# Kernel tuning notes

Hardware: AMD Instinct MI355X
Metric: run time of the kernel (lower is better)

Reference implementation:

```python
import jax, jax.numpy as jnp
import numpy as np

EPS = 1e-5
H = 16  # num_heads


def _ln(x, s, b):
    m = x.mean(-1, keepdims=True)
    v = x.var(-1, keepdims=True)
    return (x - m) / jnp.sqrt(v + EPS) * s + b


def _gru_gate(x, y, W, U, bg):
    # W, U: [3, D, D] stacked (Wr, Wz, Wg) / (Ur, Uz, Ug); torch Linear: a @ W.T
    r = jax.nn.sigmoid(y @ W[0].T + x @ U[0].T)
    z = jax.nn.sigmoid(y @ W[1].T + x @ U[1].T - bg)
    h = jnp.tanh(y @ W[2].T + (r * x) @ U[2].T)
    return (1.0 - z) * x + z * h


def setup_inputs() -> dict:
    N, L, D = 4, 1024, 1024
    hs = D // H
    rng = jax.random.key(0)
    ks = iter(jax.random.split(rng, 24))

    def xav(shape):
        sc = float(np.sqrt(2.0 / (shape[-1] + shape[-2])))
        return jax.random.normal(next(ks), shape, jnp.float32) * sc

    inp = {
        'value': jax.random.normal(next(ks), (N, L, D), jnp.float32),
        'key': jax.random.normal(next(ks), (N, L, D), jnp.float32),
        'query': jax.random.normal(next(ks), (N, L, D), jnp.float32),
        'mask': jax.random.randint(next(ks), (N, L), 0, 2).astype(jnp.int32),
        # shared-head QKV projections (head_size x head_size)
        'wq': xav((hs, hs)), 'wk': xav((hs, hs)), 'wv': xav((hs, hs)),
        'w_out': xav((D, D)), 'b_out': jnp.zeros((D,), jnp.float32),
        'fc_w': xav((D, D)), 'fc_b': jnp.zeros((D,), jnp.float32),
        'ln1_s': jnp.ones((D,), jnp.float32), 'ln1_b': jnp.zeros((D,), jnp.float32),
        'lnkv_s': jnp.ones((D,), jnp.float32), 'lnkv_b': jnp.zeros((D,), jnp.float32),
        'ln2_s': jnp.ones((D,), jnp.float32), 'ln2_b': jnp.zeros((D,), jnp.float32),
        'g1_W': xav((3, D, D)), 'g1_U': xav((3, D, D)), 'g1_bg': jnp.full((D,), 2.0, jnp.float32),
        'g2_W': xav((3, D, D)), 'g2_U': xav((3, D, D)), 'g2_bg': jnp.full((D,), 2.0, jnp.float32),
    }
    return inp


def reference(value, key, query, mask, wq, wk, wv, w_out, b_out, fc_w, fc_b,
              ln1_s, ln1_b, lnkv_s, lnkv_b, ln2_s, ln2_b,
              g1_W, g1_U, g1_bg, g2_W, g2_U, g2_bg):
    N, L, D = query.shape
    hs = D // H
    # pre-LN: query normed with norm1, value normed with norm_kv; key := normed value
    q_ = _ln(query, ln1_s, ln1_b)
    v_ = _ln(value, lnkv_s, lnkv_b)
    k_ = v_
    # shared per-head projections: [N, L, H, hs] @ W.T
    qh = q_.reshape(N, L, H, hs) @ wq.T
    kh = k_.reshape(N, L, H, hs) @ wk.T
    vh = v_.reshape(N, L, H, hs) @ wv.T
    energy = jnp.einsum('nqhd,nkhd->nhqk', qh, kh)
    energy = jnp.where(mask[:, None, None, :] == 0, jnp.float32(-1e20), energy)
    # NOTE: original scales by sqrt(embed_dim), not sqrt(head_size)
    attn = jax.nn.softmax(energy / jnp.sqrt(jnp.float32(D)), axis=-1)
    o = jnp.einsum('nhqk,nkhd->nqhd', attn, vh).reshape(N, L, D) @ w_out.T + b_out
    # GRU-gated residuals (GTrXL)
    h = _gru_gate(query, o, g1_W, g1_U, g1_bg)
    h_ = _ln(h, ln2_s, ln2_b)
    f = jax.nn.relu(h_ @ fc_w.T + fc_b)
    out = _gru_gate(h, f, g2_W, g2_U, g2_bg)
    return out, attn
```

## Files before the change

kernel.cpp:

```cpp
#include <hip/hip_runtime.h>
#include <cstdint>
#include <cstddef>

#define N_ 4
#define L_ 1024
#define D_ 1024
#define H_ 16
#define HS_ 64
#define M_ (N_*L_)
#define DD_ (D_*D_)

typedef unsigned short u16;
typedef __bf16 b16x8 __attribute__((ext_vector_type(8)));
typedef float f32x4 __attribute__((ext_vector_type(4)));

__device__ __forceinline__ float sigmoidf_(float x) { return 1.0f / (1.0f + __expf(-x)); }
__device__ __forceinline__ u16 f2bf(float f) {
    union { float f; uint32_t u; } c; c.f = f;
    uint32_t u = c.u;
    u += 0x7fffu + ((u >> 16) & 1u);
    return (u16)(u >> 16);
}

__device__ __forceinline__ void gl_lds16(const void* g, void* l) {
    auto gp = reinterpret_cast<const __attribute__((address_space(1))) unsigned int*>(
        reinterpret_cast<uintptr_t>(g));
    auto lp = reinterpret_cast<__attribute__((address_space(3))) unsigned int*>(
        reinterpret_cast<uintptr_t>(l));
    __builtin_amdgcn_global_load_lds(gp, lp, 16, 0, 0);
}

__global__ __launch_bounds__(256) void prep_weights_kernel(
    const float* __restrict__ w_out, const float* __restrict__ fc_w,
    const float* __restrict__ wq, const float* __restrict__ wk, const float* __restrict__ wv,
    const float* __restrict__ g1W, const float* __restrict__ g1U,
    const float* __restrict__ g2W, const float* __restrict__ g2U,
    u16* __restrict__ ws0) {
    u16* Wop = ws0;
    u16* Wfc = ws0 + (size_t)DD_;
    u16* WQKV = ws0 + 2 * (size_t)DD_;
    u16* G1rz = WQKV + 16384;
    u16* G1h = G1rz + 4 * (size_t)DD_;
    u16* G2rz = G1h + 2 * (size_t)DD_;
    u16* G2h = G2rz + 4 * (size_t)DD_;
    int b = blockIdx.x, t = threadIdx.x;
    const float* src; u16* dst; size_t si, di;
    if (b < 512) {
        size_t f = (size_t)b * 2048 + t * 8; src = w_out; si = f; dst = Wop; di = f;
    } else if (b < 1024) {
        size_t f = (size_t)(b - 512) * 2048 + t * 8; src = fc_w; si = f; dst = Wfc; di = f;
    } else if (b < 1030) {
        size_t f = (size_t)(b - 1024) * 2048 + t * 8;
        int which = (int)(f >> 12); size_t off = f & 4095;
        src = which == 0 ? wq : (which == 1 ? wk : wv); si = off; dst = WQKV; di = f;
    } else if (b < 3078) {
        size_t f = (size_t)(b - 1030) * 2048 + t * 8;
        size_t row = f >> 11, k = f & 2047; size_t n2 = (row >= 1024) ? 1 : 0;
        src = (k < 1024) ? (g1W + n2 * DD_) : (g1U + n2 * DD_);
        si = (row & 1023) * 1024 + (k & 1023); dst = G1rz; di = f;
    } else if (b < 4102) {
        size_t f = (size_t)(b - 3078) * 2048 + t * 8;
        size_t row = f >> 11, k = f & 2047;
        src = (k < 1024) ? (g1W + 2 * (size_t)DD_) : (g1U + 2 * (size_t)DD_);
        si = row * 1024 + (k & 1023); dst = G1h; di = f;
    } else if (b < 6150) {
        size_t f = (size_t)(b - 4102) * 2048 + t * 8;
        size_t row = f >> 11, k = f & 2047; size_t n2 = (row >= 1024) ? 1 : 0;
        src = (k < 1024) ? (g2W + n2 * DD_) : (g2U + n2 * DD_);
        si = (row & 1023) * 1024 + (k & 1023); dst = G2rz; di = f;
    } else {
        size_t f = (size_t)(b - 6150) * 2048 + t * 8;
        size_t row = f >> 11, k = f & 2047;
        src = (k < 1024) ? (g2W + 2 * (size_t)DD_) : (g2U + 2 * (size_t)DD_);
        si = row * 1024 + (k & 1023); dst = G2h; di = f;
    }
    float4 a = *(const float4*)&src[si];
    float4 b4 = *(const float4*)&src[si + 4];
    u16 o[8] = { f2bf(a.x), f2bf(a.y), f2bf(a.z), f2bf(a.w),
                 f2bf(b4.x), f2bf(b4.y), f2bf(b4.z), f2bf(b4.w) };
    *(uint4*)&dst[di] = *(uint4*)o;
}

__global__ __launch_bounds__(256) void ln_kernel(const float* __restrict__ x, u16* __restrict__ y,
                                                 const float* __restrict__ sc, const float* __restrict__ bi) {
    int row = blockIdx.x;
    const float* xr = x + (size_t)row * D_;
    int t = threadIdx.x;
    float4 v = *(const float4*)&xr[t * 4];
    float s = v.x + v.y + v.z + v.w;
    float q = v.x * v.x + v.y * v.y + v.z * v.z + v.w * v.w;
#pragma unroll
    for (int o = 32; o > 0; o >>= 1) { s += __shfl_xor(s, o); q += __shfl_xor(q, o); }
    __shared__ float ss[4], sq[4];
    int w = t >> 6;
    if ((t & 63) == 0) { ss[w] = s; sq[w] = q; }
    __syncthreads();
    s = ss[0] + ss[1] + ss[2] + ss[3];
    q = sq[0] + sq[1] + sq[2] + sq[3];
    float mean = s * (1.0f / D_);
    float var = q * (1.0f / D_) - mean * mean;
    float inv = rsqrtf(var + 1e-5f);
    float4 sv = *(const float4*)&sc[t * 4];
    float4 bv = *(const float4*)&bi[t * 4];
    u16 ov[4] = { f2bf((v.x - mean) * inv * sv.x + bv.x),
                  f2bf((v.y - mean) * inv * sv.y + bv.y),
                  f2bf((v.z - mean) * inv * sv.z + bv.z),
                  f2bf((v.w - mean) * inv * sv.w + bv.w) };
    *(ushort4*)&y[(size_t)row * D_ + t * 4] = *(ushort4*)ov;
}

__global__ __launch_bounds__(256) void proj_mfma_kernel(const u16* __restrict__ qbf,
                                                        const u16* __restrict__ vbf,
                                                        const u16* __restrict__ wqkv,
                                                        u16* __restrict__ qh, u16* __restrict__ kh,
                                                        u16* __restrict__ vt) {
    int t = threadIdx.x, w = t >> 6, l = t & 63;
    int lr = l & 15, lg = l >> 4;
    int rb = blockIdx.x, h = blockIdx.y;
    int n = rb >> 3, lbase = (rb & 7) * 128;
    const u16* wqp = wqkv;
    const u16* wkp = wqkv + 4096;
    const u16* wvp = wqkv + 8192;
    b16x8 wqf[4][2], wkf[4][2], wvf[4][2];
#pragma unroll
    for (int dt = 0; dt < 4; ++dt)
#pragma unroll
        for (int ks = 0; ks < 2; ++ks) {
            int a = (dt * 16 + lr) * 64 + ks * 32 + lg * 8;
            wqf[dt][ks] = *(const b16x8*)&wqp[a];
            wkf[dt][ks] = *(const b16x8*)&wkp[a];
            wvf[dt][ks] = *(const b16x8*)&wvp[a];
        }
#pragma unroll
    for (int rr = 0; rr < 2; ++rr) {
        int rt = w * 2 + rr;
        size_t grow = (size_t)(n * 1024 + lbase + rt * 16 + lr);
        b16x8 aq[2], av[2];
#pragma unroll
        for (int ks = 0; ks < 2; ++ks) {
            aq[ks] = *(const b16x8*)&qbf[grow * D_ + h * 64 + ks * 32 + lg * 8];
            av[ks] = *(const b16x8*)&vbf[grow * D_ + h * 64 + ks * 32 + lg * 8];
        }
#pragma unroll
        for (int dt = 0; dt < 4; ++dt) {
            f32x4 cq = (f32x4){0.f, 0.f, 0.f, 0.f};
            f32x4 ck = (f32x4){0.f, 0.f, 0.f, 0.f};
            f32x4 cv = (f32x4){0.f, 0.f, 0.f, 0.f};
            cq = __builtin_amdgcn_mfma_f32_16x16x32_bf16(aq[0], wqf[dt][0], cq, 0, 0, 0);
            cq = __builtin_amdgcn_mfma_f32_16x16x32_bf16(aq[1], wqf[dt][1], cq, 0, 0, 0);
            ck = __builtin_amdgcn_mfma_f32_16x16x32_bf16(av[0], wkf[dt][0], ck, 0, 0, 0);
            ck = __builtin_amdgcn_mfma_f32_16x16x32_bf16(av[1], wkf[dt][1], ck, 0, 0, 0);
            cv = __builtin_amdgcn_mfma_f32_16x16x32_bf16(wvf[dt][0], av[0], cv, 0, 0, 0);
            cv = __builtin_amdgcn_mfma_f32_16x16x32_bf16(wvf[dt][1], av[1], cv, 0, 0, 0);
#pragma unroll
            for (int r = 0; r < 4; ++r) {
                size_t orow = (size_t)(n * 1024 + lbase + rt * 16 + lg * 4 + r);
                qh[orow * D_ + h * 64 + dt * 16 + lr] = f2bf(cq[r]);
                kh[orow * D_ + h * 64 + dt * 16 + lr] = f2bf(ck[r]);
                vt[((size_t)(n * H_ + h) * 64 + dt * 16 + lg * 4 + r) * L_ + lbase + rt * 16 + lr] = f2bf(cv[r]);
            }
        }
    }
}

__global__ __launch_bounds__(512, 2) void qk_softmax_kernel(const u16* __restrict__ qh,
                                                            const u16* __restrict__ kh,
                                                            const int* __restrict__ mask,
                                                            float* __restrict__ attn) {
    int t = threadIdx.x;
    int w = t >> 6, l = t & 63;
    int qsub = w & 1, kq = w >> 1;
    int q0 = blockIdx.x * 32;
    int h = blockIdx.y, n = blockIdx.z;
    int lr = l & 15, lg = l >> 4;

    size_t qrow = ((size_t)(n * L_ + q0 + qsub * 16 + lr) * H_ + h) * HS_;
    b16x8 aq0 = *(const b16x8*)&qh[qrow + lg * 8];
    b16x8 aq1 = *(const b16x8*)&qh[qrow + 32 + lg * 8];

    f32x4 c[16];
#pragma unroll
    for (int i = 0; i < 16; ++i) c[i] = (f32x4){0.f, 0.f, 0.f, 0.f};

    size_t kbase = ((size_t)(n * L_ + kq * 256 + lr) * H_ + h) * HS_ + lg * 8;
#pragma unroll
    for (int kt = 0; kt < 16; ++kt) {
        const u16* kp = &kh[kbase + (size_t)kt * 16 * D_];
        b16x8 bk0 = *(const b16x8*)&kp[0];
        b16x8 bk1 = *(const b16x8*)&kp[32];
        c[kt] = __builtin_amdgcn_mfma_f32_16x16x32_bf16(aq0, bk0, c[kt], 0, 0, 0);
        c[kt] = __builtin_amdgcn_mfma_f32_16x16x32_bf16(aq1, bk1, c[kt], 0, 0, 0);
    }

    const float scl = 0.03125f;
    int kcol = kq * 256 + lr;
    float rowmax[4] = { -1e30f, -1e30f, -1e30f, -1e30f };
#pragma unroll
    for (int kt = 0; kt < 16; ++kt) {
        int mk = mask[n * L_ + kcol + kt * 16];
#pragma unroll
        for (int r = 0; r < 4; ++r) {
            float s = (mk != 0) ? c[kt][r] * scl : -1e20f;
            c[kt][r] = s;
            rowmax[r] = fmaxf(rowmax[r], s);
        }
    }
#pragma unroll
    for (int o = 8; o > 0; o >>= 1)
#pragma unroll
        for (int r = 0; r < 4; ++r) rowmax[r] = fmaxf(rowmax[r], __shfl_xor(rowmax[r], o));

    __shared__ float redA[32][4];
    __shared__ float redB[32][4];
    int qrow4 = qsub * 16 + lg * 4;
    if (lr == 0) {
#pragma unroll
        for (int r = 0; r < 4; ++r) redA[qrow4 + r][kq] = rowmax[r];
    }
    __syncthreads();
#pragma unroll
    for (int r = 0; r < 4; ++r)
        rowmax[r] = fmaxf(fmaxf(redA[qrow4 + r][0], redA[qrow4 + r][1]),
                          fmaxf(redA[qrow4 + r][2], redA[qrow4 + r][3]));
    float rowsum[4] = { 0.f, 0.f, 0.f, 0.f };
#pragma unroll
    for (int kt = 0; kt < 16; ++kt)
#pragma unroll
        for (int r = 0; r < 4; ++r) {
            float e = __expf(c[kt][r] - rowmax[r]);
            c[kt][r] = e;
            rowsum[r] += e;
        }
#pragma unroll
    for (int o = 8; o > 0; o >>= 1)
#pragma unroll
        for (int r = 0; r < 4; ++r) rowsum[r] += __shfl_xor(rowsum[r], o);
    if (lr == 0) {
#pragma unroll
        for (int r = 0; r < 4; ++r) redB[qrow4 + r][kq] = rowsum[r];
    }
    __syncthreads();
    float inv[4];
#pragma unroll
    for (int r = 0; r < 4; ++r)
        inv[r] = 1.0f / (redB[qrow4 + r][0] + redB[qrow4 + r][1] +
                         redB[qrow4 + r][2] + redB[qrow4 + r][3]);

    float* ap = attn + ((size_t)((n * H_ + h) * L_) + q0 + qrow4) * L_ + kcol;
#pragma unroll
    for (int kt = 0; kt < 16; ++kt)
#pragma unroll
        for (int r = 0; r < 4; ++r)
            ap[(size_t)r * L_ + kt * 16] = c[kt][r] * inv[r];
}

#define PLD 40
__global__ __launch_bounds__(256) void pv_mfma_kernel(const float* __restrict__ attn,
                                                      const u16* __restrict__ vt,
                                                      u16* __restrict__ o) {
    __shared__ u16 a_lds[128 * PLD];
    __shared__ u16 v_lds[64 * PLD];
    int t = threadIdx.x, w = t >> 6, l = t & 63;
    int lr = l & 15, lg = l >> 4;
    int qb = blockIdx.x * 128, h = blockIdx.y, n = blockIdx.z;
    const float* abase = attn + ((size_t)((n * H_ + h) * L_) + qb) * L_;
    const u16* vbase = vt + (size_t)(n * H_ + h) * HS_ * L_;
    f32x4 acc[4][2];
#pragma unroll
    for (int i = 0; i < 4; ++i)
#pragma unroll
        for (int j = 0; j < 2; ++j) acc[i][j] = (f32x4){0.f, 0.f, 0.f, 0.f};

    int sq = t >> 1, sk = (t & 1) * 16;
    int vd = t >> 2, vk = (t & 3) * 8;
    for (int kb = 0; kb < L_; kb += 32) {
        float va[16];
#pragma unroll
        for (int i = 0; i < 4; ++i)
            *(float4*)&va[i * 4] = *(const float4*)&abase[(size_t)sq * L_ + kb + sk + i * 4];
        b16x8 vv = *(const b16x8*)&vbase[(size_t)vd * L_ + kb + vk];
        u16 ua[16];
#pragma unroll
        for (int i = 0; i < 16; ++i) ua[i] = f2bf(va[i]);
        __syncthreads();
        *(uint4*)&a_lds[sq * PLD + sk] = *(uint4*)&ua[0];
        *(uint4*)&a_lds[sq * PLD + sk + 8] = *(uint4*)&ua[8];
        *(b16x8*)&v_lds[vd * PLD + vk] = vv;
        __syncthreads();
        b16x8 bq[2];
#pragma unroll
        for (int qt = 0; qt < 2; ++qt)
            bq[qt] = *(const b16x8*)&a_lds[(w * 32 + qt * 16 + lr) * PLD + lg * 8];
#pragma unroll
        for (int dt = 0; dt < 4; ++dt) {
            b16x8 av = *(const b16x8*)&v_lds[(dt * 16 + lr) * PLD + lg * 8];
#pragma unroll
            for (int qt = 0; qt < 2; ++qt)
                acc[dt][qt] = __builtin_amdgcn_mfma_f32_16x16x32_bf16(av, bq[qt], acc[dt][qt], 0, 0, 0);
        }
    }
#pragma unroll
    for (int dt = 0; dt < 4; ++dt)
#pragma unroll
        for (int qt = 0; qt < 2; ++qt) {
            int q = qb + w * 32 + qt * 16 + lr;
            int d = dt * 16 + lg * 4;
            u16 ov[4] = { f2bf(acc[dt][qt][0]), f2bf(acc[dt][qt][1]),
                          f2bf(acc[dt][qt][2]), f2bf(acc[dt][qt][3]) };
            *(ushort4*)&o[((size_t)(n * L_ + q) * H_ + h) * HS_ + d] = *(ushort4*)ov;
        }
}

__global__ __launch_bounds__(256) void gemm_bf16_kernel(const u16* __restrict__ A, int lda,
                                                        const u16* __restrict__ Bw, int ldb,
                                                        const float* __restrict__ bias,
                                                        float* __restrict__ C0, float* __restrict__ C1,
                                                        u16* __restrict__ Cbf, int ldc,
                                                        int K, int relu) {
    __shared__ u16 As[2][128 * 64];
    __shared__ u16 Bs[2][128 * 64];
    int t = threadIdx.x, w = t >> 6, l = t & 63;
    int wr = w >> 1, wc = w & 1;
    int m0 = blockIdx.x * 128, n0 = blockIdx.y * 128;
    int fr = l & 15, fq = l >> 4;
    int srow = l >> 3;
    int gc8 = (l & 7) ^ (srow & 7);
    const u16* Abase = A + (size_t)m0 * lda;
    const u16* Bbase = Bw + (size_t)n0 * ldb;

    f32x4 acc[4][4];
#pragma unroll
    for (int i = 0; i < 4; ++i)
#pragma unroll
        for (int j = 0; j < 4; ++j) acc[i][j] = (f32x4){0.f, 0.f, 0.f, 0.f};

    auto STAGE = [&](int buf, int kk) {
#pragma unroll
        for (int i = 0; i < 4; ++i) {
            int r0 = (i * 4 + w) * 8;
            gl_lds16(&Abase[(size_t)(r0 + srow) * lda + kk + gc8 * 8], &As[buf][r0 * 64]);
            gl_lds16(&Bbase[(size_t)(r0 + srow) * ldb + kk + gc8 * 8], &Bs[buf][r0 * 64]);
        }
    };
    STAGE(0, 0);
    const int NT = K >> 6;
    for (int kt = 0; kt < NT; ++kt) {
        int cur = kt & 1;
        if (kt + 1 < NT) {
            STAGE(cur ^ 1, (kt + 1) << 6);
            asm volatile("s_waitcnt vmcnt(8)" ::: "memory");
        } else {
            asm volatile("s_waitcnt vmcnt(0)" ::: "memory");
        }
        __builtin_amdgcn_s_barrier();
#pragma unroll
        for (int ks = 0; ks < 2; ++ks) {
            b16x8 af[4], bf[4];
#pragma unroll
            for (int i = 0; i < 4; ++i) {
                int row = wr * 64 + i * 16 + fr;
                af[i] = *(const b16x8*)&As[cur][row * 64 + (((ks * 4 + fq) ^ (fr & 7)) * 8)];
            }
#pragma unroll
            for (int j = 0; j < 4; ++j) {
                int row = wc * 64 + j * 16 + fr;
                bf[j] = *(const b16x8*)&Bs[cur][row * 64 + (((ks * 4 + fq) ^ (fr & 7)) * 8)];
            }
#pragma unroll
            for (int i = 0; i < 4; ++i)
#pragma unroll
                for (int j = 0; j < 4; ++j)
                    acc[i][j] = __builtin_amdgcn_mfma_f32_16x16x32_bf16(af[i], bf[j], acc[i][j], 0, 0, 0);
        }
        asm volatile("s_waitcnt lgkmcnt(0)" ::: "memory");
        __builtin_amdgcn_s_barrier();
    }
#pragma unroll
    for (int i = 0; i < 4; ++i) {
#pragma unroll
        for (int j = 0; j < 4; ++j) {
            int row = m0 + wr * 64 + i * 16 + fq * 4;
            int col = n0 + wc * 64 + j * 16 + fr;
            float bv = bias ? bias[col] : 0.f;
#pragma unroll
            for (int r = 0; r < 4; ++r) {
                float v = acc[i][j][r] + bv;
                if (relu) v = fmaxf(v, 0.f);
                if (Cbf) {
                    Cbf[(size_t)(row + r) * ldc + col] = f2bf(v);
                } else {
                    float* dst = (col < 1024) ? C0 : C1;
                    dst[(size_t)(row + r) * 1024 + (col & 1023)] = v;
                }
            }
        }
    }
}

__global__ __launch_bounds__(256) void gate_rz_t_kernel(const float* __restrict__ rp, float* __restrict__ zp,
                                                        const float* __restrict__ x, const float* __restrict__ bg,
                                                        u16* __restrict__ tbf) {
    int i = blockIdx.x * 256 + threadIdx.x;
    float4 r4 = ((const float4*)rp)[i];
    float4 z4 = ((const float4*)zp)[i];
    float4 x4 = ((const float4*)x)[i];
    float4 b4 = *(const float4*)&bg[(i & 255) * 4];
    u16 tv[4] = { f2bf(sigmoidf_(r4.x) * x4.x), f2bf(sigmoidf_(r4.y) * x4.y),
                  f2bf(sigmoidf_(r4.z) * x4.z), f2bf(sigmoidf_(r4.w) * x4.w) };
    float4 zz = { sigmoidf_(z4.x - b4.x), sigmoidf_(z4.y - b4.y),
                  sigmoidf_(z4.z - b4.z), sigmoidf_(z4.w - b4.w) };
    size_t f = (size_t)i * 4;
    size_t row = f >> 10, col = f & 1023;
    *(ushort4*)&tbf[row * 2048 + 1024 + col] = *(ushort4*)tv;
    ((float4*)zp)[i] = zz;
}

template<int WRH>
__global__ __launch_bounds__(256) void gate_out_kernel(const float* __restrict__ hp, const float* __restrict__ z,
                                                       const float* x, float* outf, u16* __restrict__ hbf) {
    int i = blockIdx.x * 256 + threadIdx.x;
    float4 h4 = ((const float4*)hp)[i];
    float4 z4 = ((const float4*)z)[i];
    float4 x4 = ((const float4*)x)[i];
    float4 o;
    o.x = (1.f - z4.x) * x4.x + z4.x * tanhf(h4.x);
    o.y = (1.f - z4.y) * x4.y + z4.y * tanhf(h4.y);
    o.z = (1.f - z4.z) * x4.z + z4.z * tanhf(h4.z);
    o.w = (1.f - z4.w) * x4.w + z4.w * tanhf(h4.w);
    ((float4*)outf)[i] = o;
    if (WRH) {
        u16 hv[4] = { f2bf(o.x), f2bf(o.y), f2bf(o.z), f2bf(o.w) };
        size_t f = (size_t)i * 4;
        size_t row = f >> 10, col = f & 1023;
        *(ushort4*)&hbf[row * 2048 + 1024 + col] = *(ushort4*)hv;
    }
}

__global__ __launch_bounds__(256) void cvtq_kernel(const float* __restrict__ src, u16* __restrict__ dst) {
    size_t f = ((size_t)blockIdx.x * 256 + threadIdx.x) * 8;
    float4 a = *(const float4*)&src[f];
    float4 b = *(const float4*)&src[f + 4];
    u16 o[8] = { f2bf(a.x), f2bf(a.y), f2bf(a.z), f2bf(a.w),
                 f2bf(b.x), f2bf(b.y), f2bf(b.z), f2bf(b.w) };
    size_t row = f >> 10, col = f & 1023;
    *(uint4*)&dst[row * 2048 + 1024 + col] = *(uint4*)o;
}

extern "C" void kernel_launch(void* const* d_in, const int* in_sizes, int n_in,
                              void* d_out, int out_size, void* d_ws, size_t ws_size,
                              hipStream_t stream) {
    const float* value = (const float*)d_in[0];
    const float* query = (const float*)d_in[2];
    const int* mask = (const int*)d_in[3];
    const float* wq = (const float*)d_in[4];
    const float* wk = (const float*)d_in[5];
    const float* wv = (const float*)d_in[6];
    const float* w_out = (const float*)d_in[7];
    const float* b_out = (const float*)d_in[8];
    const float* fc_w = (const float*)d_in[9];
    const float* fc_b = (const float*)d_in[10];
    const float* ln1_s = (const float*)d_in[11];
    const float* ln1_b = (const float*)d_in[12];
    const float* lnkv_s = (const float*)d_in[13];
    const float* lnkv_b = (const float*)d_in[14];
    const float* ln2_s = (const float*)d_in[15];
    const float* ln2_b = (const float*)d_in[16];
    const float* g1_W = (const float*)d_in[17];
    const float* g1_U = (const float*)d_in[18];
    const float* g1_bg = (const float*)d_in[19];
    const float* g2_W = (const float*)d_in[20];
    const float* g2_U = (const float*)d_in[21];
    const float* g2_bg = (const float*)d_in[22];

    float* out_f = (float*)d_out;
    float* attn_f = out_f + (size_t)M_ * D_;
    float* OutH = out_f;

    u16* WS = (u16*)d_ws;
    u16* Wop = WS;
    u16* Wfc = WS + (size_t)DD_;
    u16* WQKV = WS + 2 * (size_t)DD_;
    u16* G1rz = WQKV + 16384;
    u16* G1h  = G1rz + 4 * (size_t)DD_;
    u16* G2rz = G1h + 2 * (size_t)DD_;
    u16* G2h  = G2rz + 4 * (size_t)DD_;
    u16* A1   = G2h + 2 * (size_t)DD_;
    float* P0 = (float*)(A1 + 8 * (size_t)DD_ / 1);
    P0 = (float*)(A1 + (size_t)M_ * 2048);
    float* P1 = P0 + (size_t)M_ * D_;
    u16* QH  = (u16*)(P1 + (size_t)M_ * D_);
    u16* KH  = QH + (size_t)M_ * D_;
    u16* VT  = KH + (size_t)M_ * D_;
    u16* OBF = VT + (size_t)M_ * D_;
    u16* LNQ = OBF + (size_t)M_ * D_;
    u16* LNV = LNQ + (size_t)M_ * D_;
    u16* LN2 = LNV + (size_t)M_ * D_;

    const int EW_GRID = (M_ * D_ / 4) / 256;
    dim3 grid_n1024(M_ / 128, 8);
    dim3 grid_n2048(M_ / 128, 16);

    prep_weights_kernel<<<7174, 256, 0, stream>>>(w_out, fc_w, wq, wk, wv,
                                                  g1_W, g1_U, g2_W, g2_U, WS);

    ln_kernel<<<M_, 256, 0, stream>>>(query, LNQ, ln1_s, ln1_b);
    ln_kernel<<<M_, 256, 0, stream>>>(value, LNV, lnkv_s, lnkv_b);
    proj_mfma_kernel<<<dim3(32, 16), 256, 0, stream>>>(LNQ, LNV, WQKV, QH, KH, VT);
    qk_softmax_kernel<<<dim3(L_ / 32, H_, N_), 512, 0, stream>>>(QH, KH, mask, attn_f);
    cvtq_kernel<<<M_ * D_ / 2048, 256, 0, stream>>>(query, A1);
    pv_mfma_kernel<<<dim3(L_ / 128, H_, N_), 256, 0, stream>>>(attn_f, VT, OBF);
    gemm_bf16_kernel<<<grid_n1024, 256, 0, stream>>>(OBF, 1024, Wop, 1024, b_out,
                                                     nullptr, nullptr, A1, 2048, 1024, 0);

    gemm_bf16_kernel<<<grid_n2048, 256, 0, stream>>>(A1, 2048, G1rz, 2048, nullptr,
                                                     P0, P1, nullptr, 0, 2048, 0);
    gate_rz_t_kernel<<<EW_GRID, 256, 0, stream>>>(P0, P1, query, g1_bg, A1);
    gemm_bf16_kernel<<<grid_n1024, 256, 0, stream>>>(A1, 2048, G1h, 2048, nullptr,
                                                     P0, nullptr, nullptr, 0, 2048, 0);
    gate_out_kernel<1><<<EW_GRID, 256, 0, stream>>>(P0, P1, query, OutH, A1);

    ln_kernel<<<M_, 256, 0, stream>>>(OutH, LN2, ln2_s, ln2_b);
    gemm_bf16_kernel<<<grid_n1024, 256, 0, stream>>>(LN2, 1024, Wfc, 1024, fc_b,
                                                     nullptr, nullptr, A1, 2048, 1024, 1);

    gemm_bf16_kernel<<<grid_n2048, 256, 0, stream>>>(A1, 2048, G2rz, 2048, nullptr,
                                                     P0, P1, nullptr, 0, 2048, 0);
    gate_rz_t_kernel<<<EW_GRID, 256, 0, stream>>>(P0, P1, OutH, g2_bg, A1);
    gemm_bf16_kernel<<<grid_n1024, 256, 0, stream>>>(A1, 2048, G2h, 2048, nullptr,
                                                     P0, nullptr, nullptr, 0, 2048, 0);
    gate_out_kernel<0><<<EW_GRID, 256, 0, stream>>>(P0, P1, OutH, out_f, nullptr);
}
```

Measured before the change: 466.1 us.

## Fuse PV into softmax kernel and GRU gate elementwise into GEMM epilogues

The attention PV product now runs in the QK-softmax kernel, reading bf16 probabilities from LDS instead of re-reading the fp32 attention matrix from global memory. The GRU gate elementwise kernels (sigmoid/tanh gating) are folded into the GEMM epilogues, and the GEMM takes its two K-halves from separate buffers, so concatenated staging and fp32 intermediates go away. The softmax kernel's LDS grows to about 64KB for the P tile, and launch bounds rise to 4 blocks per CU, which may not be achievable and may limit occupancy.

```diff
diff --git a/kernel.cpp b/kernel.cpp
--- a/kernel.cpp
+++ b/kernel.cpp
@@ -9,6 +9,7 @@
 #define HS_ 64
 #define M_ (N_*L_)
 #define DD_ (D_*D_)
+#define MD_ ((size_t)M_*D_)
 
 typedef unsigned short u16;
 typedef __bf16 b16x8 __attribute__((ext_vector_type(8)));
@@ -109,6 +110,15 @@
     *(ushort4*)&y[(size_t)row * D_ + t * 4] = *(ushort4*)ov;
 }
 
+__global__ __launch_bounds__(256) void cvtq_kernel(const float* __restrict__ src, u16* __restrict__ dst) {
+    size_t f = ((size_t)blockIdx.x * 256 + threadIdx.x) * 8;
+    float4 a = *(const float4*)&src[f];
+    float4 b = *(const float4*)&src[f + 4];
+    u16 o[8] = { f2bf(a.x), f2bf(a.y), f2bf(a.z), f2bf(a.w),
+                 f2bf(b.x), f2bf(b.y), f2bf(b.z), f2bf(b.w) };
+    *(uint4*)&dst[f] = *(uint4*)o;
+}
+
 __global__ __launch_bounds__(256) void proj_mfma_kernel(const u16* __restrict__ qbf,
                                                         const u16* __restrict__ vbf,
                                                         const u16* __restrict__ wqkv,
@@ -163,10 +173,16 @@
     }
 }
 
-__global__ __launch_bounds__(512, 2) void qk_softmax_kernel(const u16* __restrict__ qh,
-                                                            const u16* __restrict__ kh,
-                                                            const int* __restrict__ mask,
-                                                            float* __restrict__ attn) {
+#define PSTR 1032
+__global__ __launch_bounds__(512, 4) void qk_pv_kernel(const u16* __restrict__ qh,
+                                                       const u16* __restrict__ kh,
+                                                       const u16* __restrict__ vt,
+                                                       const int* __restrict__ mask,
+                                                       float* __restrict__ attn,
+                                                       u16* __restrict__ obf) {
+    __shared__ u16 P_lds[32 * PSTR];
+    __shared__ float redA[32][4];
+    __shared__ float redB[32][4];
     int t = threadIdx.x;
     int w = t >> 6, l = t & 63;
     int qsub = w & 1, kq = w >> 1;
@@ -210,8 +226,6 @@
 #pragma unroll
         for (int r = 0; r < 4; ++r) rowmax[r] = fmaxf(rowmax[r], __shfl_xor(rowmax[r], o));
 
-    __shared__ float redA[32][4];
-    __shared__ float redB[32][4];
     int qrow4 = qsub * 16 + lg * 4;
     if (lr == 0) {
 #pragma unroll
@@ -250,73 +264,40 @@
 #pragma unroll
     for (int kt = 0; kt < 16; ++kt)
 #pragma unroll
-        for (int r = 0; r < 4; ++r)
-            ap[(size_t)r * L_ + kt * 16] = c[kt][r] * inv[r];
-}
-
-#define PLD 40
-__global__ __launch_bounds__(256) void pv_mfma_kernel(const float* __restrict__ attn,
-                                                      const u16* __restrict__ vt,
-                                                      u16* __restrict__ o) {
-    __shared__ u16 a_lds[128 * PLD];
-    __shared__ u16 v_lds[64 * PLD];
-    int t = threadIdx.x, w = t >> 6, l = t & 63;
-    int lr = l & 15, lg = l >> 4;
-    int qb = blockIdx.x * 128, h = blockIdx.y, n = blockIdx.z;
-    const float* abase = attn + ((size_t)((n * H_ + h) * L_) + qb) * L_;
-    const u16* vbase = vt + (size_t)(n * H_ + h) * HS_ * L_;
-    f32x4 acc[4][2];
-#pragma unroll
-    for (int i = 0; i < 4; ++i)
-#pragma unroll
-        for (int j = 0; j < 2; ++j) acc[i][j] = (f32x4){0.f, 0.f, 0.f, 0.f};
-
-    int sq = t >> 1, sk = (t & 1) * 16;
-    int vd = t >> 2, vk = (t & 3) * 8;
-    for (int kb = 0; kb < L_; kb += 32) {
-        float va[16];
-#pragma unroll
-        for (int i = 0; i < 4; ++i)
-            *(float4*)&va[i * 4] = *(const float4*)&abase[(size_t)sq * L_ + kb + sk + i * 4];
-        b16x8 vv = *(const b16x8*)&vbase[(size_t)vd * L_ + kb + vk];
-        u16 ua[16];
-#pragma unroll
-        for (int i = 0; i < 16; ++i) ua[i] = f2bf(va[i]);
-        __syncthreads();
-        *(uint4*)&a_lds[sq * PLD + sk] = *(uint4*)&ua[0];
-        *(uint4*)&a_lds[sq * PLD + sk + 8] = *(uint4*)&ua[8];
-        *(b16x8*)&v_lds[vd * PLD + vk] = vv;
-        __syncthreads();
-        b16x8 bq[2];
-#pragma unroll
-        for (int qt = 0; qt < 2; ++qt)
-            bq[qt] = *(const b16x8*)&a_lds[(w * 32 + qt * 16 + lr) * PLD + lg * 8];
-#pragma unroll
-        for (int dt = 0; dt < 4; ++dt) {
-            b16x8 av = *(const b16x8*)&v_lds[(dt * 16 + lr) * PLD + lg * 8];
-#pragma unroll
-            for (int qt = 0; qt < 2; ++qt)
-                acc[dt][qt] = __builtin_amdgcn_mfma_f32_16x16x32_bf16(av, bq[qt], acc[dt][qt], 0, 0, 0);
-        }
-    }
-#pragma unroll
-    for (int dt = 0; dt < 4; ++dt)
-#pragma unroll
-        for (int qt = 0; qt < 2; ++qt) {
-            int q = qb + w * 32 + qt * 16 + lr;
-            int d = dt * 16 + lg * 4;
-            u16 ov[4] = { f2bf(acc[dt][qt][0]), f2bf(acc[dt][qt][1]),
-                          f2bf(acc[dt][qt][2]), f2bf(acc[dt][qt][3]) };
-            *(ushort4*)&o[((size_t)(n * L_ + q) * H_ + h) * HS_ + d] = *(ushort4*)ov;
-        }
-}
-
-__global__ __launch_bounds__(256) void gemm_bf16_kernel(const u16* __restrict__ A, int lda,
-                                                        const u16* __restrict__ Bw, int ldb,
-                                                        const float* __restrict__ bias,
-                                                        float* __restrict__ C0, float* __restrict__ C1,
-                                                        u16* __restrict__ Cbf, int ldc,
-                                                        int K, int relu) {
+        for (int r = 0; r < 4; ++r) {
+            float val = c[kt][r] * inv[r];
+            ap[(size_t)r * L_ + kt * 16] = val;
+            P_lds[(size_t)(qrow4 + r) * PSTR + kcol + kt * 16] = f2bf(val);
+        }
+    __syncthreads();
+
+    int dg = kq;
+    const u16* vb = vt + ((size_t)(n * H_ + h) * 64 + dg * 16 + lr) * L_;
+    const u16* prow = &P_lds[(size_t)(qsub * 16 + lr) * PSTR];
+    f32x4 acc = (f32x4){0.f, 0.f, 0.f, 0.f};
+#pragma unroll
+    for (int ks = 0; ks < 32; ++ks) {
+        b16x8 a = *(const b16x8*)&prow[ks * 32 + lg * 8];
+        b16x8 b = *(const b16x8*)&vb[ks * 32 + lg * 8];
+        acc = __builtin_amdgcn_mfma_f32_16x16x32_bf16(a, b, acc, 0, 0, 0);
+    }
+#pragma unroll
+    for (int r = 0; r < 4; ++r) {
+        size_t q = (size_t)(n * L_ + q0 + qsub * 16 + lg * 4 + r);
+        obf[q * D_ + h * 64 + dg * 16 + lr] = f2bf(acc[r]);
+    }
+}
+
+template<int MODE, int RELU, int WRH>
+__global__ __launch_bounds__(256) void gemm_fused_kernel(const u16* __restrict__ A0,
+                                                         const u16* __restrict__ A1h,
+                                                         const u16* __restrict__ Bw,
+                                                         const float* __restrict__ bias,
+                                                         const float* __restrict__ xf,
+                                                         float* __restrict__ Z,
+                                                         u16* __restrict__ Cbf,
+                                                         float* __restrict__ outf,
+                                                         int K) {
     __shared__ u16 As[2][128 * 64];
     __shared__ u16 Bs[2][128 * 64];
     int t = threadIdx.x, w = t >> 6, l = t & 63;
@@ -325,8 +306,7 @@
     int fr = l & 15, fq = l >> 4;
     int srow = l >> 3;
     int gc8 = (l & 7) ^ (srow & 7);
-    const u16* Abase = A + (size_t)m0 * lda;
-    const u16* Bbase = Bw + (size_t)n0 * ldb;
+    const u16* Bbase = Bw + (size_t)n0 * K;
 
     f32x4 acc[4][4];
 #pragma unroll
@@ -335,11 +315,13 @@
         for (int j = 0; j < 4; ++j) acc[i][j] = (f32x4){0.f, 0.f, 0.f, 0.f};
 
     auto STAGE = [&](int buf, int kk) {
+        const u16* Asrc = (kk < 1024) ? A0 : A1h;
+        int kc = kk & 1023;
 #pragma unroll
         for (int i = 0; i < 4; ++i) {
             int r0 = (i * 4 + w) * 8;
-            gl_lds16(&Abase[(size_t)(r0 + srow) * lda + kk + gc8 * 8], &As[buf][r0 * 64]);
-            gl_lds16(&Bbase[(size_t)(r0 + srow) * ldb + kk + gc8 * 8], &Bs[buf][r0 * 64]);
+            gl_lds16(&Asrc[(size_t)(m0 + r0 + srow) * 1024 + kc + gc8 * 8], &As[buf][r0 * 64]);
+            gl_lds16(&Bbase[(size_t)(r0 + srow) * K + kk + gc8 * 8], &Bs[buf][r0 * 64]);
         }
     };
     STAGE(0, 0);
@@ -381,69 +363,27 @@
         for (int j = 0; j < 4; ++j) {
             int row = m0 + wr * 64 + i * 16 + fq * 4;
             int col = n0 + wc * 64 + j * 16 + fr;
-            float bv = bias ? bias[col] : 0.f;
+            int c1 = col & 1023;
 #pragma unroll
             for (int r = 0; r < 4; ++r) {
-                float v = acc[i][j][r] + bv;
-                if (relu) v = fmaxf(v, 0.f);
-                if (Cbf) {
-                    Cbf[(size_t)(row + r) * ldc + col] = f2bf(v);
+                float v = acc[i][j][r];
+                size_t off = (size_t)(row + r) * 1024 + c1;
+                if (MODE == 0) {
+                    v += bias[col];
+                    if (RELU) v = fmaxf(v, 0.f);
+                    Cbf[off] = f2bf(v);
+                } else if (MODE == 1) {
+                    if (col < 1024) Cbf[off] = f2bf(sigmoidf_(v) * xf[off]);
+                    else            Z[off] = sigmoidf_(v - bias[c1]);
                 } else {
-                    float* dst = (col < 1024) ? C0 : C1;
-                    dst[(size_t)(row + r) * 1024 + (col & 1023)] = v;
+                    float z = Z[off];
+                    float o = (1.f - z) * xf[off] + z * tanhf(v);
+                    outf[off] = o;
+                    if (WRH) Cbf[off] = f2bf(o);
                 }
             }
         }
     }
-}
-
-__global__ __launch_bounds__(256) void gate_rz_t_kernel(const float* __restrict__ rp, float* __restrict__ zp,
-                                                        const float* __restrict__ x, const float* __restrict__ bg,
-                                                        u16* __restrict__ tbf) {
-    int i = blockIdx.x * 256 + threadIdx.x;
-    float4 r4 = ((const float4*)rp)[i];
-    float4 z4 = ((const float4*)zp)[i];
-    float4 x4 = ((const float4*)x)[i];
-    float4 b4 = *(const float4*)&bg[(i & 255) * 4];
-    u16 tv[4] = { f2bf(sigmoidf_(r4.x) * x4.x), f2bf(sigmoidf_(r4.y) * x4.y),
-                  f2bf(sigmoidf_(r4.z) * x4.z), f2bf(sigmoidf_(r4.w) * x4.w) };
-    float4 zz = { sigmoidf_(z4.x - b4.x), sigmoidf_(z4.y - b4.y),
-                  sigmoidf_(z4.z - b4.z), sigmoidf_(z4.w - b4.w) };
-    size_t f = (size_t)i * 4;
-    size_t row = f >> 10, col = f & 1023;
-    *(ushort4*)&tbf[row * 2048 + 1024 + col] = *(ushort4*)tv;
-    ((float4*)zp)[i] = zz;
-}
-
-template<int WRH>
-__global__ __launch_bounds__(256) void gate_out_kernel(const float* __restrict__ hp, const float* __restrict__ z,
-                                                       const float* x, float* outf, u16* __restrict__ hbf) {
-    int i = blockIdx.x * 256 + threadIdx.x;
-    float4 h4 = ((const float4*)hp)[i];
-    float4 z4 = ((const float4*)z)[i];
-    float4 x4 = ((const float4*)x)[i];
-    float4 o;
-    o.x = (1.f - z4.x) * x4.x + z4.x * tanhf(h4.x);
-    o.y = (1.f - z4.y) * x4.y + z4.y * tanhf(h4.y);
-    o.z = (1.f - z4.z) * x4.z + z4.z * tanhf(h4.z);
-    o.w = (1.f - z4.w) * x4.w + z4.w * tanhf(h4.w);
-    ((float4*)outf)[i] = o;
-    if (WRH) {
-        u16 hv[4] = { f2bf(o.x), f2bf(o.y), f2bf(o.z), f2bf(o.w) };
-        size_t f = (size_t)i * 4;
-        size_t row = f >> 10, col = f & 1023;
-        *(ushort4*)&hbf[row * 2048 + 1024 + col] = *(ushort4*)hv;
-    }
-}
-
-__global__ __launch_bounds__(256) void cvtq_kernel(const float* __restrict__ src, u16* __restrict__ dst) {
-    size_t f = ((size_t)blockIdx.x * 256 + threadIdx.x) * 8;
-    float4 a = *(const float4*)&src[f];
-    float4 b = *(const float4*)&src[f + 4];
-    u16 o[8] = { f2bf(a.x), f2bf(a.y), f2bf(a.z), f2bf(a.w),
-                 f2bf(b.x), f2bf(b.y), f2bf(b.z), f2bf(b.w) };
-    size_t row = f >> 10, col = f & 1023;
-    *(uint4*)&dst[row * 2048 + 1024 + col] = *(uint4*)o;
 }
 
 extern "C" void kernel_launch(void* const* d_in, const int* in_sizes, int n_in,
@@ -473,7 +413,7 @@
     const float* g2_bg = (const float*)d_in[22];
 
     float* out_f = (float*)d_out;
-    float* attn_f = out_f + (size_t)M_ * D_;
+    float* attn_f = out_f + MD_;
     float* OutH = out_f;
 
     u16* WS = (u16*)d_ws;
@@ -484,19 +424,20 @@
     u16* G1h  = G1rz + 4 * (size_t)DD_;
     u16* G2rz = G1h + 2 * (size_t)DD_;
     u16* G2h  = G2rz + 4 * (size_t)DD_;
-    u16* A1   = G2h + 2 * (size_t)DD_;
-    float* P0 = (float*)(A1 + 8 * (size_t)DD_ / 1);
-    P0 = (float*)(A1 + (size_t)M_ * 2048);
-    float* P1 = P0 + (size_t)M_ * D_;
-    u16* QH  = (u16*)(P1 + (size_t)M_ * D_);
-    u16* KH  = QH + (size_t)M_ * D_;
-    u16* VT  = KH + (size_t)M_ * D_;
-    u16* OBF = VT + (size_t)M_ * D_;
-    u16* LNQ = OBF + (size_t)M_ * D_;
-    u16* LNV = LNQ + (size_t)M_ * D_;
-    u16* LN2 = LNV + (size_t)M_ * D_;
-
-    const int EW_GRID = (M_ * D_ / 4) / 256;
+    u16* Y    = G2h + 2 * (size_t)DD_;
+    u16* Xq   = Y + MD_;
+    u16* T1   = Xq + MD_;
+    u16* Hb   = T1 + MD_;
+    u16* F    = Hb + MD_;
+    u16* QH   = F + MD_;
+    u16* KH   = QH + MD_;
+    u16* VT   = KH + MD_;
+    u16* OBF  = VT + MD_;
+    u16* LNQ  = OBF + MD_;
+    u16* LNV  = LNQ + MD_;
+    u16* LN2  = LNV + MD_;
+    float* Z  = (float*)(LN2 + MD_);
+
     dim3 grid_n1024(M_ / 128, 8);
     dim3 grid_n2048(M_ / 128, 16);
 
@@ -506,27 +447,19 @@
     ln_kernel<<<M_, 256, 0, stream>>>(query, LNQ, ln1_s, ln1_b);
     ln_kernel<<<M_, 256, 0, stream>>>(value, LNV, lnkv_s, lnkv_b);
     proj_mfma_kernel<<<dim3(32, 16), 256, 0, stream>>>(LNQ, LNV, WQKV, QH, KH, VT);
-    qk_softmax_kernel<<<dim3(L_ / 32, H_, N_), 512, 0, stream>>>(QH, KH, mask, attn_f);
-    cvtq_kernel<<<M_ * D_ / 2048, 256, 0, stream>>>(query, A1);
-    pv_mfma_kernel<<<dim3(L_ / 128, H_, N_), 256, 0, stream>>>(attn_f, VT, OBF);
-    gemm_bf16_kernel<<<grid_n1024, 256, 0, stream>>>(OBF, 1024, Wop, 1024, b_out,
-                                                     nullptr, nullptr, A1, 2048, 1024, 0);
-
-    gemm_bf16_kernel<<<grid_n2048, 256, 0, stream>>>(A1, 2048, G1rz, 2048, nullptr,
-                                                     P0, P1, nullptr, 0, 2048, 0);
-    gate_rz_t_kernel<<<EW_GRID, 256, 0, stream>>>(P0, P1, query, g1_bg, A1);
-    gemm_bf16_kernel<<<grid_n1024, 256, 0, stream>>>(A1, 2048, G1h, 2048, nullptr,
-                                                     P0, nullptr, nullptr, 0, 2048, 0);
-    gate_out_kernel<1><<<EW_GRID, 256, 0, stream>>>(P0, P1, query, OutH, A1);
-
+    cvtq_kernel<<<M_ * D_ / 2048, 256, 0, stream>>>(query, Xq);
+    qk_pv_kernel<<<dim3(L_ / 32, H_, N_), 512, 0, stream>>>(QH, KH, VT, mask, attn_f, OBF);
+    gemm_fused_kernel<0, 0, 0><<<grid_n1024, 256, 0, stream>>>(OBF, nullptr, Wop, b_out,
+                                                               nullptr, nullptr, Y, nullptr, 1024);
+    gemm_fused_kernel<1, 0, 0><<<grid_n2048, 256, 0, stream>>>(Y, Xq, G1rz, g1_bg,
+                                                               query, Z, T1, nullptr, 2048);
+    gemm_fused_kernel<2, 0, 1><<<grid_n1024, 256, 0, stream>>>(Y, T1, G1h, nullptr,
+                                                               query, Z, Hb, OutH, 2048);
     ln_kernel<<<M_, 256, 0, stream>>>(OutH, LN2, ln2_s, ln2_b);
-    gemm_bf16_kernel<<<grid_n1024, 256, 0, stream>>>(LN2, 1024, Wfc, 1024, fc_b,
-                                                     nullptr, nullptr, A1, 2048, 1024, 1);
-
-    gemm_bf16_kernel<<<grid_n2048, 256, 0, stream>>>(A1, 2048, G2rz, 2048, nullptr,
-                                                     P0, P1, nullptr, 0, 2048, 0);
-    gate_rz_t_kernel<<<EW_GRID, 256, 0, stream>>>(P0, P1, OutH, g2_bg, A1);
-    gemm_bf16_kernel<<<grid_n1024, 256, 0, stream>>>(A1, 2048, G2h, 2048, nullptr,
-                                                     P0, nullptr, nullptr, 0, 2048, 0);
-    gate_out_kernel<0><<<EW_GRID, 256, 0, stream>>>(P0, P1, OutH, out_f, nullptr);
-}
+    gemm_fused_kernel<0, 1, 0><<<grid_n1024, 256, 0, stream>>>(LN2, nullptr, Wfc, fc_b,
+                                                               nullptr, nullptr, F, nullptr, 1024);
+    gemm_fused_kernel<1, 0, 0><<<grid_n2048, 256, 0, stream>>>(F, Hb, G2rz, g2_bg,
+                                                               OutH, Z, T1, nullptr, 2048);
+    gemm_fused_kernel<2, 0, 0><<<grid_n1024, 256, 0, stream>>>(F, T1, G2h, nullptr,
+                                                               OutH, Z, nullptr, out_f, 2048);
+}
```

Result: faster. 441.1 us (-5.4%).
